# Kernel optimization log

Hardware: AMD Instinct MI355X
Metric: run time of the kernel (lower is better)

Reference implementation:

```python
import jax, jax.numpy as jnp
import numpy as np

B, N, C, CI = 2, 8192, 128, 128
K_SAMP, K_NN = 120, 30  # sampling_ratio, nn_nb
GN_GROUPS, GN_CH = 2, 128
EPS = 1e-5


def setup_inputs() -> dict:
    key = jax.random.key(0)
    ks = jax.random.split(key, 7)
    return {
        "points": jax.random.normal(ks[0], (B, N, 3), jnp.float32),
        "feature": jax.random.normal(ks[1], (B, N, C), jnp.float32),
        "instance_feature": jax.random.normal(ks[2], (B, N, CI), jnp.float32),
        "kpam_w1": jax.random.normal(ks[3], (K_NN, K_NN), jnp.float32) * 0.1,
        "kpam_w2": jax.random.normal(ks[4], (K_NN, K_NN), jnp.float32) * 0.1,
        "conv_w": jax.random.normal(ks[5], (128, 131), jnp.float32) * 0.05,
        "gn_gamma": jnp.ones((GN_CH,), jnp.float32),
        "gn_beta": jnp.zeros((GN_CH,), jnp.float32),
        "mlp_w": jax.random.normal(ks[6], (3, 256), jnp.float32) * 0.05,
        "mlp_b": jnp.zeros((3,), jnp.float32),
    }


def _key_indices(n):
    # replicate torch module: np.random.seed(1234); shuffle(arange(N)); take first 120
    rs = np.random.RandomState(1234)
    l = np.arange(n)
    rs.shuffle(l)
    return jnp.asarray(l[:K_SAMP])


def reference(points, feature, instance_feature, kpam_w1, kpam_w2,
              conv_w, gn_gamma, gn_beta, mlp_w, mlp_b):
    Bv, Nv, _ = points.shape
    idx = _key_indices(Nv)                              # [120] static indices
    key_points = points[:, idx]                         # [B,120,3]
    feat_s = feature[:, idx]                            # [B,120,128]
    inst_s = instance_feature[:, idx]                   # [B,120,CI]

    # cos_dist: -(1 - cos) == cos - 1
    fn = instance_feature / jnp.linalg.norm(instance_feature, axis=-1, keepdims=True)
    gn = inst_s / jnp.linalg.norm(inst_s, axis=-1, keepdims=True)
    dist = jnp.einsum('bnc,bkc->bnk', fn, gn) - 1.0     # [B,N,120]

    topk_dist, topk_idx = jax.lax.top_k(dist, K_NN)     # [B,N,30]

    gather = jax.vmap(lambda tab, ix: tab[ix])          # tab [120,D], ix [N,30]
    topk_kp = gather(key_points, topk_idx)              # [B,N,30,3]
    topk_feat = gather(feat_s, topk_idx)                # [B,N,30,128]

    direction = topk_kp - points[:, :, None, :]         # [B,N,30,3]
    x = jnp.concatenate([topk_feat, direction], axis=3) # [B,N,30,131]

    # KPAM: two 1x1 conv1d over k-channel of topk_dist, softmax over k
    a = jax.nn.relu(jnp.einsum('bnk,ok->bno', topk_dist, kpam_w1))
    a = jnp.einsum('bno,po->bnp', a, kpam_w2)
    attn = jax.nn.softmax(a, axis=2)[..., None]         # [B,N,30,1]
    fa = attn * x                                       # [B,N,30,131]

    # conv1: 1x1 Conv2d 131->128 on layout [B,131,30,N]
    y = jnp.einsum('bnkc,oc->bokn', fa, conv_w)         # [B,128,30,N]

    # GroupNorm(2, 128)
    yg = y.reshape(Bv, GN_GROUPS, GN_CH // GN_GROUPS, K_NN, Nv)
    mu = yg.mean(axis=(2, 3, 4), keepdims=True)
    var = yg.var(axis=(2, 3, 4), keepdims=True)
    yg = (yg - mu) * jax.lax.rsqrt(var + EPS)
    y = yg.reshape(Bv, GN_CH, K_NN, Nv)
    y = y * gn_gamma[None, :, None, None] + gn_beta[None, :, None, None]
    y = jnp.where(y >= 0, y, 0.2 * y)                   # LeakyReLU(0.2)

    y = y.max(axis=2)                                   # max over k -> [B,128,N]
    feat_cat = jnp.concatenate([y, feature.transpose(0, 2, 1)], axis=1)  # [B,256,N]

    offsets = jnp.einsum('bcn,oc->bon', feat_cat, mlp_w) + mlp_b[None, :, None]
    return offsets  # [B,3,N]
```

## Files before the change

### kernel.cpp

```cpp
#include <hip/hip_runtime.h>

#define Bv   2
#define Nv   8192
#define Cv   128
#define KSv  120
#define KNNv 30

namespace mtns {
struct MTState { unsigned mt[624]; int mti; };
constexpr void mt_seed(MTState& s, unsigned seed) {
  for (int pos = 0; pos < 624; ++pos) {
    s.mt[pos] = seed;
    seed = 1812433253u * (seed ^ (seed >> 30)) + (unsigned)pos + 1u;
  }
  s.mti = 624;
}
constexpr unsigned mt_next(MTState& s) {
  if (s.mti >= 624) {
    for (int i = 0; i < 624; ++i) {
      unsigned y = (s.mt[i] & 0x80000000u) | (s.mt[(i + 1) % 624] & 0x7fffffffu);
      unsigned v = s.mt[(i + 397) % 624] ^ (y >> 1);
      s.mt[i] = (y & 1u) ? (v ^ 0x9908b0dfu) : v;
    }
    s.mti = 0;
  }
  unsigned y = s.mt[s.mti++];
  y ^= y >> 11;
  y ^= (y << 7) & 0x9d2c5680u;
  y ^= (y << 15) & 0xefc60000u;
  y ^= y >> 18;
  return y;
}
struct IdxTable { int v[KSv]; };
constexpr IdxTable make_idx() {
  MTState st{};
  mt_seed(st, 1234u);
  int arr[Nv] = {};
  for (int i = 0; i < Nv; ++i) arr[i] = i;
  for (int i = Nv - 1; i > 0; --i) {
    unsigned mask = (unsigned)i;
    mask |= mask >> 1; mask |= mask >> 2; mask |= mask >> 4;
    mask |= mask >> 8; mask |= mask >> 16;
    unsigned j = 0;
    do { j = mt_next(st) & mask; } while (j > (unsigned)i);
    int tmp = arr[i]; arr[i] = arr[(int)j]; arr[(int)j] = tmp;
  }
  IdxTable out{};
  for (int k = 0; k < KSv; ++k) out.v[k] = arr[k];
  return out;
}
}

__constant__ mtns::IdxTable IDX = mtns::make_idx();

__device__ __forceinline__ float wave_sum(float v) {
  #pragma unroll
  for (int m = 32; m; m >>= 1) v += __shfl_xor(v, m);
  return v;
}

__device__ __forceinline__ float opaque(float x) {
  asm volatile("" : "+v"(x));
  return x;
}

__device__ __forceinline__ float rdf(float v, int k) {
  return __int_as_float(__builtin_amdgcn_readlane(__float_as_int(v), k));
}
__device__ __forceinline__ int rdi(int v, int k) {
  return __builtin_amdgcn_readlane(v, k);
}

__device__ __forceinline__ float npyv_reduce(const float4* a) {
  float4 h0, h1, h;
  h0.x = a[0].x + a[2].x; h0.y = a[0].y + a[2].y;
  h0.z = a[0].z + a[2].z; h0.w = a[0].w + a[2].w;
  h1.x = a[1].x + a[3].x; h1.y = a[1].y + a[3].y;
  h1.z = a[1].z + a[3].z; h1.w = a[1].w + a[3].w;
  h.x = h0.x + h1.x; h.y = h0.y + h1.y; h.z = h0.z + h1.z; h.w = h0.w + h1.w;
  float sx = h.x + h.z;
  float sy = h.y + h.w;
  return sx + sy;
}

__global__ void k0_prepare(const float* __restrict__ points,
                           const float* __restrict__ feature,
                           const float* __restrict__ inst,
                           const float* __restrict__ conv_w,
                           float* __restrict__ gn32W,
                           float* __restrict__ GW,
                           int* __restrict__ counter) {
  int bk = blockIdx.x;
  int b = bk / KSv, kp = bk % KSv;
  int jg = IDX.v[kp];
  int t = threadIdx.x;
  if (bk == 0 && t == 0) *counter = 0;
  __shared__ float featS[Cv];
  __shared__ float rowS[Cv];
  __shared__ float ptS[3];
  __shared__ float nAcc[8];
  __shared__ float nrmSh;
  long rowi = (long)b * Nv + jg;
  float iv = inst[rowi * Cv + t];
  rowS[t] = iv;
  featS[t] = feature[rowi * Cv + t];
  if (t < 3) ptS[t] = points[rowi * 3 + t];
  __syncthreads();
  if (t < 8) {
    float x0 = rowS[t];
    float acc = opaque(x0 * x0);
    #pragma unroll
    for (int i = 1; i < 16; ++i) {
      float xv = rowS[8 * i + t];
      acc = acc + opaque(xv * xv);
    }
    nAcc[t] = acc;
  }
  __syncthreads();
  if (t == 0) {
    float res = ((nAcc[0] + nAcc[1]) + (nAcc[2] + nAcc[3])) +
                ((nAcc[4] + nAcc[5]) + (nAcc[6] + nAcc[7]));
    nrmSh = sqrtf(res);
  }
  __syncthreads();
  gn32W[(b * KSv + kp) * Cv + t] = iv / nrmSh;
  const float* cw = conv_w + t * 131;
  float acc = 0.f;
  #pragma unroll 8
  for (int c = 0; c < Cv; ++c) acc = fmaf(featS[c], cw[c], acc);
  acc = fmaf(ptS[0], cw[128], fmaf(ptS[1], cw[129], fmaf(ptS[2], cw[130], acc)));
  GW[(b * KSv + kp) * Cv + t] = acc;
}

__global__ __launch_bounds__(512, 4) void k2_main(
    const float* __restrict__ points,
    const float* __restrict__ inst,
    const float* __restrict__ w1,
    const float* __restrict__ w2,
    const float* __restrict__ conv_w,
    const float* __restrict__ gamma,
    const float* __restrict__ gn32,
    const float* __restrict__ GW,
    float* __restrict__ Msel,
    float2* __restrict__ part,
    int* __restrict__ counter,
    float2* __restrict__ stats) {
  __shared__ float4 gnS[KSv * 32];
  __shared__ float sc[8 * 512];
  __shared__ float2 partS[16];
  __shared__ int lastFlag;

  int bid = blockIdx.x;
  int b = bid >> 9;
  int chunk = bid & 511;
  int tid = threadIdx.x;
  int w = tid >> 6, l = tid & 63;

  const float4* gnG = (const float4*)(gn32 + (long)b * KSv * Cv);
  for (int i = tid; i < KSv * 32; i += 512) {
    int kp = i >> 5, c4 = i & 31;
    gnS[kp * 32 + (c4 ^ (kp & 31))] = gnG[i];
  }
  __syncthreads();

  float* wb = sc + w * 512;
  float* fnA = wb;
  float* fnB = wb + 128;
  float* dsA = wb + 256;
  float* dsB = wb + 384;
  float* tvA = dsA; int* tiA = (int*)(dsA + 32);
  float* tvB = dsB; int* tiB = (int*)(dsB + 32);

  int c0 = 2 * l;
  int nA = chunk * 16 + 2 * w;
  long rowA = (long)b * Nv + nA;
  long rowB = rowA + 1;
  const float* Gb = GW + (long)b * KSv * Cv;
  const float NINF = -__builtin_inff();

  float2 ivA = *(const float2*)(inst + rowA * Cv + c0);
  float2 ivB = *(const float2*)(inst + rowB * Cv + c0);
  ((float2*)fnA)[l] = ivA;
  ((float2*)fnB)[l] = ivB;
  __builtin_amdgcn_wave_barrier();

  float acc = 0.f;
  if (l < 16) {
    const float* xr = (l < 8) ? fnA : fnB;
    int j = l & 7;
    float x0 = xr[j];
    acc = opaque(x0 * x0);
    #pragma unroll
    for (int i = 1; i < 16; ++i) {
      float xv = xr[8 * i + j];
      acc = acc + opaque(xv * xv);
    }
  }
  float nrmA = sqrtf(((rdf(acc, 0) + rdf(acc, 1)) + (rdf(acc, 2) + rdf(acc, 3))) +
                     ((rdf(acc, 4) + rdf(acc, 5)) + (rdf(acc, 6) + rdf(acc, 7))));
  float nrmB = sqrtf(((rdf(acc, 8) + rdf(acc, 9)) + (rdf(acc, 10) + rdf(acc, 11))) +
                     ((rdf(acc, 12) + rdf(acc, 13)) + (rdf(acc, 14) + rdf(acc, 15))));
  __builtin_amdgcn_wave_barrier();
  float2 fA2, fB2;
  fA2.x = ivA.x / nrmA; fA2.y = ivA.y / nrmA;
  fB2.x = ivB.x / nrmB; fB2.y = ivB.y / nrmB;
  ((float2*)fnA)[l] = fA2;
  ((float2*)fnB)[l] = fB2;
  __builtin_amdgcn_wave_barrier();

  const float4* fA4 = (const float4*)fnA;
  const float4* fB4 = (const float4*)fnB;
  int sw = l & 31;
  const float4* g0r = gnS + l * 32;
  int r1 = 64 + l; if (r1 > KSv - 1) r1 = KSv - 1;
  const float4* g1r = gnS + r1 * 32;
  float4 aA0[4], aA1[4], aB0[4], aB1[4];
  #pragma unroll
  for (int i = 0; i < 4; ++i) {
    aA0[i] = float4{0,0,0,0}; aA1[i] = float4{0,0,0,0};
    aB0[i] = float4{0,0,0,0}; aB1[i] = float4{0,0,0,0};
  }
  #pragma unroll 4
  for (int c4 = 0; c4 < 32; ++c4) {
    float4 fa = fA4[c4];
    float4 fb = fB4[c4];
    float4 g0 = g0r[c4 ^ sw];
    float4 g1 = g1r[c4 ^ sw];
    int m = c4 & 3;
    aA0[m].x = fmaf(g0.x, fa.x, aA0[m].x); aA0[m].y = fmaf(g0.y, fa.y, aA0[m].y);
    aA0[m].z = fmaf(g0.z, fa.z, aA0[m].z); aA0[m].w = fmaf(g0.w, fa.w, aA0[m].w);
    aB0[m].x = fmaf(g0.x, fb.x, aB0[m].x); aB0[m].y = fmaf(g0.y, fb.y, aB0[m].y);
    aB0[m].z = fmaf(g0.z, fb.z, aB0[m].z); aB0[m].w = fmaf(g0.w, fb.w, aB0[m].w);
    aA1[m].x = fmaf(g1.x, fa.x, aA1[m].x); aA1[m].y = fmaf(g1.y, fa.y, aA1[m].y);
    aA1[m].z = fmaf(g1.z, fa.z, aA1[m].z); aA1[m].w = fmaf(g1.w, fa.w, aA1[m].w);
    aB1[m].x = fmaf(g1.x, fb.x, aB1[m].x); aB1[m].y = fmaf(g1.y, fb.y, aB1[m].y);
    aB1[m].z = fmaf(g1.z, fb.z, aB1[m].z); aB1[m].w = fmaf(g1.w, fb.w, aB1[m].w);
  }
  float d0A = npyv_reduce(aA0) - 1.0f;
  float d1A = npyv_reduce(aA1) - 1.0f;
  float d0B = npyv_reduce(aB0) - 1.0f;
  float d1B = npyv_reduce(aB1) - 1.0f;

  dsA[l] = d0A;
  dsB[l] = d0B;
  if (l < 56) { dsA[64 + l] = d1A; dsB[64 + l] = d1B; }
  __builtin_amdgcn_wave_barrier();

  float d1Ar = (l < 56) ? d1A : NINF;
  float d1Br = (l < 56) ? d1B : NINF;
  int rk0A = 0, rk1A = 0, rk0B = 0, rk1B = 0;
  const float4* dvA = (const float4*)dsA;
  const float4* dvB = (const float4*)dsB;
  int t1 = 64 + l;
  #pragma unroll 5
  for (int j4 = 0; j4 < KSv / 4; ++j4) {
    float4 wA = dvA[j4];
    float4 wB = dvB[j4];
    int base = j4 * 4;
    rk0A += (wA.x > d0A) || (wA.x == d0A && (base + 0) < l);
    rk0A += (wA.y > d0A) || (wA.y == d0A && (base + 1) < l);
    rk0A += (wA.z > d0A) || (wA.z == d0A && (base + 2) < l);
    rk0A += (wA.w > d0A) || (wA.w == d0A && (base + 3) < l);
    rk1A += (wA.x > d1Ar) || (wA.x == d1Ar && (base + 0) < t1);
    rk1A += (wA.y > d1Ar) || (wA.y == d1Ar && (base + 1) < t1);
    rk1A += (wA.z > d1Ar) || (wA.z == d1Ar && (base + 2) < t1);
    rk1A += (wA.w > d1Ar) || (wA.w == d1Ar && (base + 3) < t1);
    rk0B += (wB.x > d0B) || (wB.x == d0B && (base + 0) < l);
    rk0B += (wB.y > d0B) || (wB.y == d0B && (base + 1) < l);
    rk0B += (wB.z > d0B) || (wB.z == d0B && (base + 2) < l);
    rk0B += (wB.w > d0B) || (wB.w == d0B && (base + 3) < l);
    rk1B += (wB.x > d1Br) || (wB.x == d1Br && (base + 0) < t1);
    rk1B += (wB.y > d1Br) || (wB.y == d1Br && (base + 1) < t1);
    rk1B += (wB.z > d1Br) || (wB.z == d1Br && (base + 2) < t1);
    rk1B += (wB.w > d1Br) || (wB.w == d1Br && (base + 3) < t1);
  }
  __builtin_amdgcn_wave_barrier();
  if (rk0A < KNNv) { tvA[rk0A] = d0A; tiA[rk0A] = l; }
  if (l < 56 && rk1A < KNNv) { tvA[rk1A] = d1A; tiA[rk1A] = t1; }
  if (rk0B < KNNv) { tvB[rk0B] = d0B; tiB[rk0B] = l; }
  if (l < 56 && rk1B < KNNv) { tvB[rk1B] = d1B; tiB[rk1B] = t1; }
  __builtin_amdgcn_wave_barrier();
  float mytvA = 0.f, mytvB = 0.f;
  int mytiA = 0, mytiB = 0;
  if (l < KNNv) {
    mytvA = tvA[l]; mytiA = tiA[l];
    mytvB = tvB[l]; mytiB = tiB[l];
  }

  float aA = 0.f, aB = 0.f;
  if (l < KNNv) {
    const float* w1r = w1 + l * KNNv;
    #pragma unroll 6
    for (int k = 0; k < KNNv; ++k) {
      float w1k = w1r[k];
      aA = fmaf(rdf(mytvA, k), w1k, aA);
      aB = fmaf(rdf(mytvB, k), w1k, aB);
    }
    aA = fmaxf(aA, 0.f);
    aB = fmaxf(aB, 0.f);
  }
  float a2A = NINF, a2B = NINF;
  if (l < KNNv) {
    const float* w2r = w2 + l * KNNv;
    float sA2 = 0.f, sB2 = 0.f;
    #pragma unroll 6
    for (int o = 0; o < KNNv; ++o) {
      float w2o = w2r[o];
      sA2 = fmaf(rdf(aA, o), w2o, sA2);
      sB2 = fmaf(rdf(aB, o), w2o, sB2);
    }
    a2A = sA2; a2B = sB2;
  }

  float mA = a2A, mB = a2B;
  #pragma unroll
  for (int msk = 32; msk; msk >>= 1) {
    mA = fmaxf(mA, __shfl_xor(mA, msk));
    mB = fmaxf(mB, __shfl_xor(mB, msk));
  }
  float evA = (l < KNNv) ? __expf(a2A - mA) : 0.f;
  float evB = (l < KNNv) ? __expf(a2B - mB) : 0.f;
  float invA = 1.0f / wave_sum(evA);
  float invB = 1.0f / wave_sum(evB);
  float atpA = evA * invA;
  float atpB = evB * invB;

  float pA0 = points[rowA * 3 + 0], pA1 = points[rowA * 3 + 1],
        pA2 = points[rowA * 3 + 2];
  float pB0 = points[rowB * 3 + 0], pB1 = points[rowB * 3 + 1],
        pB2 = points[rowB * 3 + 2];
  int c1 = c0 + 1;
  float cwa0 = conv_w[c0 * 131 + 128], cwb0 = conv_w[c0 * 131 + 129],
        cwc0 = conv_w[c0 * 131 + 130];
  float cwa1 = conv_w[c1 * 131 + 128], cwb1 = conv_w[c1 * 131 + 129],
        cwc1 = conv_w[c1 * 131 + 130];
  float pwA0 = fmaf(pA0, cwa0, fmaf(pA1, cwb0, pA2 * cwc0));
  float pwA1 = fmaf(pA0, cwa1, fmaf(pA1, cwb1, pA2 * cwc1));
  float pwB0 = fmaf(pB0, cwa0, fmaf(pB1, cwb0, pB2 * cwc0));
  float pwB1 = fmaf(pB0, cwa1, fmaf(pB1, cwb1, pB2 * cwc1));
  float mxA0 = NINF, mnA0 = -NINF, mxA1 = NINF, mnA1 = -NINF;
  float mxB0 = NINF, mnB0 = -NINF, mxB1 = NINF, mnB1 = -NINF;
  float sA = 0.f, qA = 0.f, sB = 0.f, qB = 0.f;
  #pragma unroll 5
  for (int k = 0; k < KNNv; ++k) {
    float akA = rdf(atpA, k);
    float akB = rdf(atpB, k);
    int jkA = rdi(mytiA, k);
    int jkB = rdi(mytiB, k);
    float2 gA = *(const float2*)(Gb + jkA * Cv + c0);
    float2 gB = *(const float2*)(Gb + jkB * Cv + c0);
    float yA0 = akA * (gA.x - pwA0);
    float yA1 = akA * (gA.y - pwA1);
    float yB0 = akB * (gB.x - pwB0);
    float yB1 = akB * (gB.y - pwB1);
    mxA0 = fmaxf(mxA0, yA0); mnA0 = fminf(mnA0, yA0);
    mxA1 = fmaxf(mxA1, yA1); mnA1 = fminf(mnA1, yA1);
    mxB0 = fmaxf(mxB0, yB0); mnB0 = fminf(mnB0, yB0);
    mxB1 = fmaxf(mxB1, yB1); mnB1 = fminf(mnB1, yB1);
    sA += yA0 + yA1;
    qA = fmaf(yA0, yA0, fmaf(yA1, yA1, qA));
    sB += yB0 + yB1;
    qB = fmaf(yB0, yB0, fmaf(yB1, yB1, qB));
  }
  float ga0 = gamma[c0], ga1 = gamma[c1];
  float2 mselA, mselB;
  mselA.x = (ga0 >= 0.f) ? mxA0 : mnA0;
  mselA.y = (ga1 >= 0.f) ? mxA1 : mnA1;
  mselB.x = (ga0 >= 0.f) ? mxB0 : mnB0;
  mselB.y = (ga1 >= 0.f) ? mxB1 : mnB1;
  *(float2*)(Msel + rowA * Cv + c0) = mselA;
  *(float2*)(Msel + rowB * Cv + c0) = mselB;

  float sg = sA + sB, qg = qA + qB;
  #pragma unroll
  for (int msk = 16; msk; msk >>= 1) {
    sg += __shfl_xor(sg, msk);
    qg += __shfl_xor(qg, msk);
  }
  if ((l & 31) == 0) partS[w * 2 + (l >> 5)] = make_float2(sg, qg);
  __syncthreads();
  if (tid == 0) {
    float s0 = 0.f, q0 = 0.f, s1 = 0.f, q1 = 0.f;
    #pragma unroll
    for (int wv = 0; wv < 8; ++wv) {
      s0 += partS[wv * 2].x;     q0 += partS[wv * 2].y;
      s1 += partS[wv * 2 + 1].x; q1 += partS[wv * 2 + 1].y;
    }
    part[bid * 2 + 0] = make_float2(s0, q0);
    part[bid * 2 + 1] = make_float2(s1, q1);
    __threadfence();
    int old = atomicAdd(counter, 1);
    lastFlag = (old == (int)gridDim.x - 1);
  }
  __syncthreads();
  if (lastFlag && w < 4) {
    int bb = w >> 1, g = w & 1;
    double s = 0.0, q = 0.0;
    #pragma unroll
    for (int i = 0; i < 8; ++i) {
      float2 p = part[(bb * 512 + l + 64 * i) * 2 + g];
      s += (double)p.x;
      q += (double)p.y;
    }
    #pragma unroll
    for (int msk = 32; msk; msk >>= 1) {
      s += __shfl_xor(s, msk);
      q += __shfl_xor(q, msk);
    }
    if (l == 0) {
      const double cnt = 64.0 * 30.0 * 8192.0;
      double mu = s / cnt;
      double var = q / cnt - mu * mu;
      stats[bb * 2 + g] = make_float2((float)mu, (float)(1.0 / sqrt(var + 1e-5)));
    }
  }
}

__global__ __launch_bounds__(256) void k4_out(
    const float* __restrict__ feature,
    const float* __restrict__ gamma,
    const float* __restrict__ beta,
    const float* __restrict__ mlp_w,
    const float* __restrict__ mlp_b,
    const float* __restrict__ Msel,
    const float2* __restrict__ stats,
    float* __restrict__ out) {
  int rr = threadIdx.x >> 7;
  int t = threadIdx.x & 127;
  long row = (long)blockIdx.x * 2 + rr;
  int b = (int)(row >> 13), n = (int)(row & (Nv - 1));
  int g = t >> 6;
  float2 st = stats[b * 2 + g];
  float gam = gamma[t], bet = beta[t];
  float M = Msel[row * Cv + t];
  float yv = fmaf((M - st.x) * st.y, gam, bet);
  yv = (yv >= 0.f) ? yv : 0.2f * yv;
  float fv = feature[row * Cv + t];
  float o0 = yv * mlp_w[0 * 256 + t] + fv * mlp_w[0 * 256 + 128 + t];
  float o1 = yv * mlp_w[1 * 256 + t] + fv * mlp_w[1 * 256 + 128 + t];
  float o2 = yv * mlp_w[2 * 256 + t] + fv * mlp_w[2 * 256 + 128 + t];
  o0 = wave_sum(o0);
  o1 = wave_sum(o1);
  o2 = wave_sum(o2);
  __shared__ float red[2][2][3];
  if ((t & 63) == 0) {
    red[rr][t >> 6][0] = o0; red[rr][t >> 6][1] = o1; red[rr][t >> 6][2] = o2;
  }
  __syncthreads();
  if (t < 3)
    out[(long)b * 3 * Nv + (long)t * Nv + n] =
        red[rr][0][t] + red[rr][1][t] + mlp_b[t];
}

extern "C" void kernel_launch(void* const* d_in, const int* in_sizes, int n_in,
                              void* d_out, int out_size, void* d_ws, size_t ws_size,
                              hipStream_t stream) {
  const float* points  = (const float*)d_in[0];
  const float* feature = (const float*)d_in[1];
  const float* inst    = (const float*)d_in[2];
  const float* w1      = (const float*)d_in[3];
  const float* w2      = (const float*)d_in[4];
  const float* conv_w  = (const float*)d_in[5];
  const float* gamma   = (const float*)d_in[6];
  const float* beta    = (const float*)d_in[7];
  const float* mlp_w   = (const float*)d_in[8];
  const float* mlp_b   = (const float*)d_in[9];
  float* out = (float*)d_out;

  char* ws = (char*)d_ws;
  float* gn32   = (float*)(ws);
  float* GW     = (float*)(ws + 122880);
  float* Msel   = (float*)(ws + 245760);
  float2* part  = (float2*)(ws + 8634368);
  int* counter  = (int*)(ws + 8650752);
  float2* stats = (float2*)(ws + 8650816);

  k0_prepare<<<dim3(Bv * KSv), dim3(128), 0, stream>>>(points, feature, inst,
                                                       conv_w, gn32, GW, counter);
  k2_main<<<dim3(1024), dim3(512), 0, stream>>>(points, inst, w1, w2, conv_w,
                                                gamma, gn32, GW, Msel, part,
                                                counter, stats);
  k4_out<<<dim3(Bv * Nv / 2), dim3(256), 0, stream>>>(feature, gamma, beta,
                                                      mlp_w, mlp_b, Msel,
                                                      stats, out);
}
```

Measured before the change: 172.9 us.

## Fuse prepare, main and output kernels into one cooperative grid-synced kernel

Merges the three launches into a single cooperative kernel of 256 blocks that uses grid.sync between the key-point preparation, the main top-k/attention/conv phase, and the GroupNorm+MLP output phase. Each block now handles 64 points in four passes, keeps the selected max/min values in shared memory instead of writing Msel to global memory, and computes its GroupNorm stats redundantly. Top-k ranking is rewritten to compare packed 64-bit sortable keys via readlane. This removes launch overhead and the Msel round trip, but lowers the grid to 256 blocks at two blocks per CU and adds two grid-wide barriers.

```diff
diff --git a/kernel.cpp b/kernel.cpp
--- a/kernel.cpp
+++ b/kernel.cpp
@@ -1,4 +1,7 @@
 #include <hip/hip_runtime.h>
+#include <hip/hip_cooperative_groups.h>
+
+namespace cg = cooperative_groups;
 
 #define Bv   2
 #define Nv   8192
@@ -70,6 +73,18 @@
 __device__ __forceinline__ int rdi(int v, int k) {
   return __builtin_amdgcn_readlane(v, k);
 }
+__device__ __forceinline__ unsigned long long rdull(unsigned long long v, int k) {
+  unsigned lo = (unsigned)__builtin_amdgcn_readlane((int)(unsigned)(v & 0xFFFFFFFFull), k);
+  unsigned hi = (unsigned)__builtin_amdgcn_readlane((int)(unsigned)(v >> 32), k);
+  return (((unsigned long long)hi) << 32) | lo;
+}
+
+__device__ __forceinline__ unsigned long long mkkey(float d, int t) {
+  unsigned u = __float_as_uint(d);
+  unsigned m = (unsigned)((int)u >> 31);
+  unsigned o = u ^ (m | 0x80000000u);
+  return (((unsigned long long)o) << 7) | (unsigned)(119 - t);
+}
 
 __device__ __forceinline__ float npyv_reduce(const float4* a) {
   float4 h0, h1, h;
@@ -83,79 +98,81 @@
   return sx + sy;
 }
 
-__global__ void k0_prepare(const float* __restrict__ points,
-                           const float* __restrict__ feature,
-                           const float* __restrict__ inst,
-                           const float* __restrict__ conv_w,
-                           float* __restrict__ gn32W,
-                           float* __restrict__ GW,
-                           int* __restrict__ counter) {
-  int bk = blockIdx.x;
-  int b = bk / KSv, kp = bk % KSv;
-  int jg = IDX.v[kp];
-  int t = threadIdx.x;
-  if (bk == 0 && t == 0) *counter = 0;
-  __shared__ float featS[Cv];
-  __shared__ float rowS[Cv];
-  __shared__ float ptS[3];
-  __shared__ float nAcc[8];
-  __shared__ float nrmSh;
-  long rowi = (long)b * Nv + jg;
-  float iv = inst[rowi * Cv + t];
-  rowS[t] = iv;
-  featS[t] = feature[rowi * Cv + t];
-  if (t < 3) ptS[t] = points[rowi * 3 + t];
-  __syncthreads();
-  if (t < 8) {
-    float x0 = rowS[t];
-    float acc = opaque(x0 * x0);
-    #pragma unroll
-    for (int i = 1; i < 16; ++i) {
-      float xv = rowS[8 * i + t];
-      acc = acc + opaque(xv * xv);
-    }
-    nAcc[t] = acc;
-  }
-  __syncthreads();
-  if (t == 0) {
-    float res = ((nAcc[0] + nAcc[1]) + (nAcc[2] + nAcc[3])) +
-                ((nAcc[4] + nAcc[5]) + (nAcc[6] + nAcc[7]));
-    nrmSh = sqrtf(res);
-  }
-  __syncthreads();
-  gn32W[(b * KSv + kp) * Cv + t] = iv / nrmSh;
-  const float* cw = conv_w + t * 131;
-  float acc = 0.f;
-  #pragma unroll 8
-  for (int c = 0; c < Cv; ++c) acc = fmaf(featS[c], cw[c], acc);
-  acc = fmaf(ptS[0], cw[128], fmaf(ptS[1], cw[129], fmaf(ptS[2], cw[130], acc)));
-  GW[(b * KSv + kp) * Cv + t] = acc;
-}
-
-__global__ __launch_bounds__(512, 4) void k2_main(
+__global__ __launch_bounds__(512, 2) void k_all(
     const float* __restrict__ points,
+    const float* __restrict__ feature,
     const float* __restrict__ inst,
     const float* __restrict__ w1,
     const float* __restrict__ w2,
     const float* __restrict__ conv_w,
     const float* __restrict__ gamma,
-    const float* __restrict__ gn32,
-    const float* __restrict__ GW,
-    float* __restrict__ Msel,
+    const float* __restrict__ beta,
+    const float* __restrict__ mlp_w,
+    const float* __restrict__ mlp_b,
+    float* __restrict__ gn32,
+    float* __restrict__ GW,
     float2* __restrict__ part,
-    int* __restrict__ counter,
-    float2* __restrict__ stats) {
+    float* __restrict__ out) {
   __shared__ float4 gnS[KSv * 32];
-  __shared__ float sc[8 * 512];
+  __shared__ float sc[8 * 384];
+  __shared__ float2 mselS[8][8][64];
   __shared__ float2 partS[16];
-  __shared__ int lastFlag;
+  __shared__ float2 statsS[2];
 
   int bid = blockIdx.x;
-  int b = bid >> 9;
-  int chunk = bid & 511;
   int tid = threadIdx.x;
   int w = tid >> 6, l = tid & 63;
-
+  cg::grid_group grid = cg::this_grid();
+
+  if (bid < Bv * KSv) {
+    int b0 = bid / KSv, kp = bid % KSv;
+    int jg = IDX.v[kp];
+    float* rowS = sc;
+    float* featS = sc + 128;
+    float* ptS = sc + 256;
+    float* nAcc = sc + 260;
+    float* nrmP = sc + 268;
+    long rowi = (long)b0 * Nv + jg;
+    if (tid < Cv) {
+      rowS[tid] = inst[rowi * Cv + tid];
+      featS[tid] = feature[rowi * Cv + tid];
+      if (tid < 3) ptS[tid] = points[rowi * 3 + tid];
+    }
+    __syncthreads();
+    if (tid < 8) {
+      float x0 = rowS[tid];
+      float acc = opaque(x0 * x0);
+      #pragma unroll
+      for (int i = 1; i < 16; ++i) {
+        float xv = rowS[8 * i + tid];
+        acc = acc + opaque(xv * xv);
+      }
+      nAcc[tid] = acc;
+    }
+    __syncthreads();
+    if (tid == 0) {
+      float res = ((nAcc[0] + nAcc[1]) + (nAcc[2] + nAcc[3])) +
+                  ((nAcc[4] + nAcc[5]) + (nAcc[6] + nAcc[7]));
+      nrmP[0] = sqrtf(res);
+    }
+    __syncthreads();
+    if (tid < Cv) {
+      float iv = rowS[tid];
+      gn32[(b0 * KSv + kp) * Cv + tid] = iv / nrmP[0];
+      const float* cw = conv_w + tid * 131;
+      float acc = 0.f;
+      #pragma unroll 8
+      for (int c = 0; c < Cv; ++c) acc = fmaf(featS[c], cw[c], acc);
+      acc = fmaf(ptS[0], cw[128],
+                 fmaf(ptS[1], cw[129], fmaf(ptS[2], cw[130], acc)));
+      GW[(b0 * KSv + kp) * Cv + tid] = acc;
+    }
+  }
+  __threadfence();
+  grid.sync();
+
+  int b = bid >> 7;
+  int blocal = bid & 127;
   const float4* gnG = (const float4*)(gn32 + (long)b * KSv * Cv);
   for (int i = tid; i < KSv * 32; i += 512) {
     int kp = i >> 5, c4 = i & 31;
@@ -163,215 +180,200 @@
   }
   __syncthreads();
 
-  float* wb = sc + w * 512;
+  float* wb = sc + w * 384;
   float* fnA = wb;
   float* fnB = wb + 128;
-  float* dsA = wb + 256;
-  float* dsB = wb + 384;
-  float* tvA = dsA; int* tiA = (int*)(dsA + 32);
-  float* tvB = dsB; int* tiB = (int*)(dsB + 32);
-
-  int c0 = 2 * l;
-  int nA = chunk * 16 + 2 * w;
-  long rowA = (long)b * Nv + nA;
-  long rowB = rowA + 1;
-  const float* Gb = GW + (long)b * KSv * Cv;
-  const float NINF = -__builtin_inff();
-
-  float2 ivA = *(const float2*)(inst + rowA * Cv + c0);
-  float2 ivB = *(const float2*)(inst + rowB * Cv + c0);
-  ((float2*)fnA)[l] = ivA;
-  ((float2*)fnB)[l] = ivB;
-  __builtin_amdgcn_wave_barrier();
-
-  float acc = 0.f;
-  if (l < 16) {
-    const float* xr = (l < 8) ? fnA : fnB;
-    int j = l & 7;
-    float x0 = xr[j];
-    acc = opaque(x0 * x0);
-    #pragma unroll
-    for (int i = 1; i < 16; ++i) {
-      float xv = xr[8 * i + j];
-      acc = acc + opaque(xv * xv);
-    }
-  }
-  float nrmA = sqrtf(((rdf(acc, 0) + rdf(acc, 1)) + (rdf(acc, 2) + rdf(acc, 3))) +
-                     ((rdf(acc, 4) + rdf(acc, 5)) + (rdf(acc, 6) + rdf(acc, 7))));
-  float nrmB = sqrtf(((rdf(acc, 8) + rdf(acc, 9)) + (rdf(acc, 10) + rdf(acc, 11))) +
-                     ((rdf(acc, 12) + rdf(acc, 13)) + (rdf(acc, 14) + rdf(acc, 15))));
-  __builtin_amdgcn_wave_barrier();
-  float2 fA2, fB2;
-  fA2.x = ivA.x / nrmA; fA2.y = ivA.y / nrmA;
-  fB2.x = ivB.x / nrmB; fB2.y = ivB.y / nrmB;
-  ((float2*)fnA)[l] = fA2;
-  ((float2*)fnB)[l] = fB2;
-  __builtin_amdgcn_wave_barrier();
-
-  const float4* fA4 = (const float4*)fnA;
-  const float4* fB4 = (const float4*)fnB;
-  int sw = l & 31;
-  const float4* g0r = gnS + l * 32;
-  int r1 = 64 + l; if (r1 > KSv - 1) r1 = KSv - 1;
-  const float4* g1r = gnS + r1 * 32;
-  float4 aA0[4], aA1[4], aB0[4], aB1[4];
-  #pragma unroll
-  for (int i = 0; i < 4; ++i) {
-    aA0[i] = float4{0,0,0,0}; aA1[i] = float4{0,0,0,0};
-    aB0[i] = float4{0,0,0,0}; aB1[i] = float4{0,0,0,0};
-  }
-  #pragma unroll 4
-  for (int c4 = 0; c4 < 32; ++c4) {
-    float4 fa = fA4[c4];
-    float4 fb = fB4[c4];
-    float4 g0 = g0r[c4 ^ sw];
-    float4 g1 = g1r[c4 ^ sw];
-    int m = c4 & 3;
-    aA0[m].x = fmaf(g0.x, fa.x, aA0[m].x); aA0[m].y = fmaf(g0.y, fa.y, aA0[m].y);
-    aA0[m].z = fmaf(g0.z, fa.z, aA0[m].z); aA0[m].w = fmaf(g0.w, fa.w, aA0[m].w);
-    aB0[m].x = fmaf(g0.x, fb.x, aB0[m].x); aB0[m].y = fmaf(g0.y, fb.y, aB0[m].y);
-    aB0[m].z = fmaf(g0.z, fb.z, aB0[m].z); aB0[m].w = fmaf(g0.w, fb.w, aB0[m].w);
-    aA1[m].x = fmaf(g1.x, fa.x, aA1[m].x); aA1[m].y = fmaf(g1.y, fa.y, aA1[m].y);
-    aA1[m].z = fmaf(g1.z, fa.z, aA1[m].z); aA1[m].w = fmaf(g1.w, fa.w, aA1[m].w);
-    aB1[m].x = fmaf(g1.x, fb.x, aB1[m].x); aB1[m].y = fmaf(g1.y, fb.y, aB1[m].y);
-    aB1[m].z = fmaf(g1.z, fb.z, aB1[m].z); aB1[m].w = fmaf(g1.w, fb.w, aB1[m].w);
-  }
-  float d0A = npyv_reduce(aA0) - 1.0f;
-  float d1A = npyv_reduce(aA1) - 1.0f;
-  float d0B = npyv_reduce(aB0) - 1.0f;
-  float d1B = npyv_reduce(aB1) - 1.0f;
-
-  dsA[l] = d0A;
-  dsB[l] = d0B;
-  if (l < 56) { dsA[64 + l] = d1A; dsB[64 + l] = d1B; }
-  __builtin_amdgcn_wave_barrier();
-
-  float d1Ar = (l < 56) ? d1A : NINF;
-  float d1Br = (l < 56) ? d1B : NINF;
-  int rk0A = 0, rk1A = 0, rk0B = 0, rk1B = 0;
-  const float4* dvA = (const float4*)dsA;
-  const float4* dvB = (const float4*)dsB;
-  int t1 = 64 + l;
-  #pragma unroll 5
-  for (int j4 = 0; j4 < KSv / 4; ++j4) {
-    float4 wA = dvA[j4];
-    float4 wB = dvB[j4];
-    int base = j4 * 4;
-    rk0A += (wA.x > d0A) || (wA.x == d0A && (base + 0) < l);
-    rk0A += (wA.y > d0A) || (wA.y == d0A && (base + 1) < l);
-    rk0A += (wA.z > d0A) || (wA.z == d0A && (base + 2) < l);
-    rk0A += (wA.w > d0A) || (wA.w == d0A && (base + 3) < l);
-    rk1A += (wA.x > d1Ar) || (wA.x == d1Ar && (base + 0) < t1);
-    rk1A += (wA.y > d1Ar) || (wA.y == d1Ar && (base + 1) < t1);
-    rk1A += (wA.z > d1Ar) || (wA.z == d1Ar && (base + 2) < t1);
-    rk1A += (wA.w > d1Ar) || (wA.w == d1Ar && (base + 3) < t1);
-    rk0B += (wB.x > d0B) || (wB.x == d0B && (base + 0) < l);
-    rk0B += (wB.y > d0B) || (wB.y == d0B && (base + 1) < l);
-    rk0B += (wB.z > d0B) || (wB.z == d0B && (base + 2) < l);
-    rk0B += (wB.w > d0B) || (wB.w == d0B && (base + 3) < l);
-    rk1B += (wB.x > d1Br) || (wB.x == d1Br && (base + 0) < t1);
-    rk1B += (wB.y > d1Br) || (wB.y == d1Br && (base + 1) < t1);
-    rk1B += (wB.z > d1Br) || (wB.z == d1Br && (base + 2) < t1);
-    rk1B += (wB.w > d1Br) || (wB.w == d1Br && (base + 3) < t1);
-  }
-  __builtin_amdgcn_wave_barrier();
-  if (rk0A < KNNv) { tvA[rk0A] = d0A; tiA[rk0A] = l; }
-  if (l < 56 && rk1A < KNNv) { tvA[rk1A] = d1A; tiA[rk1A] = t1; }
-  if (rk0B < KNNv) { tvB[rk0B] = d0B; tiB[rk0B] = l; }
-  if (l < 56 && rk1B < KNNv) { tvB[rk1B] = d1B; tiB[rk1B] = t1; }
-  __builtin_amdgcn_wave_barrier();
-  float mytvA = 0.f, mytvB = 0.f;
-  int mytiA = 0, mytiB = 0;
-  if (l < KNNv) {
-    mytvA = tvA[l]; mytiA = tiA[l];
-    mytvB = tvB[l]; mytiB = tiB[l];
-  }
-
-  float aA = 0.f, aB = 0.f;
-  if (l < KNNv) {
-    const float* w1r = w1 + l * KNNv;
-    #pragma unroll 6
-    for (int k = 0; k < KNNv; ++k) {
-      float w1k = w1r[k];
-      aA = fmaf(rdf(mytvA, k), w1k, aA);
-      aB = fmaf(rdf(mytvB, k), w1k, aB);
-    }
-    aA = fmaxf(aA, 0.f);
-    aB = fmaxf(aB, 0.f);
-  }
-  float a2A = NINF, a2B = NINF;
-  if (l < KNNv) {
-    const float* w2r = w2 + l * KNNv;
-    float sA2 = 0.f, sB2 = 0.f;
-    #pragma unroll 6
-    for (int o = 0; o < KNNv; ++o) {
-      float w2o = w2r[o];
-      sA2 = fmaf(rdf(aA, o), w2o, sA2);
-      sB2 = fmaf(rdf(aB, o), w2o, sB2);
-    }
-    a2A = sA2; a2B = sB2;
-  }
-
-  float mA = a2A, mB = a2B;
-  #pragma unroll
-  for (int msk = 32; msk; msk >>= 1) {
-    mA = fmaxf(mA, __shfl_xor(mA, msk));
-    mB = fmaxf(mB, __shfl_xor(mB, msk));
-  }
-  float evA = (l < KNNv) ? __expf(a2A - mA) : 0.f;
-  float evB = (l < KNNv) ? __expf(a2B - mB) : 0.f;
-  float invA = 1.0f / wave_sum(evA);
-  float invB = 1.0f / wave_sum(evB);
-  float atpA = evA * invA;
-  float atpB = evB * invB;
-
-  float pA0 = points[rowA * 3 + 0], pA1 = points[rowA * 3 + 1],
-        pA2 = points[rowA * 3 + 2];
-  float pB0 = points[rowB * 3 + 0], pB1 = points[rowB * 3 + 1],
-        pB2 = points[rowB * 3 + 2];
-  int c1 = c0 + 1;
+  float* tvA = wb + 256; int* tiA = (int*)(wb + 288);
+  float* tvB = wb + 320; int* tiB = (int*)(wb + 352);
+
+  int c0 = 2 * l, c1 = 2 * l + 1;
+  float ga0 = gamma[c0], ga1 = gamma[c1];
   float cwa0 = conv_w[c0 * 131 + 128], cwb0 = conv_w[c0 * 131 + 129],
         cwc0 = conv_w[c0 * 131 + 130];
   float cwa1 = conv_w[c1 * 131 + 128], cwb1 = conv_w[c1 * 131 + 129],
         cwc1 = conv_w[c1 * 131 + 130];
-  float pwA0 = fmaf(pA0, cwa0, fmaf(pA1, cwb0, pA2 * cwc0));
-  float pwA1 = fmaf(pA0, cwa1, fmaf(pA1, cwb1, pA2 * cwc1));
-  float pwB0 = fmaf(pB0, cwa0, fmaf(pB1, cwb0, pB2 * cwc0));
-  float pwB1 = fmaf(pB0, cwa1, fmaf(pB1, cwb1, pB2 * cwc1));
-  float mxA0 = NINF, mnA0 = -NINF, mxA1 = NINF, mnA1 = -NINF;
-  float mxB0 = NINF, mnB0 = -NINF, mxB1 = NINF, mnB1 = -NINF;
-  float sA = 0.f, qA = 0.f, sB = 0.f, qB = 0.f;
-  #pragma unroll 5
-  for (int k = 0; k < KNNv; ++k) {
-    float akA = rdf(atpA, k);
-    float akB = rdf(atpB, k);
-    int jkA = rdi(mytiA, k);
-    int jkB = rdi(mytiB, k);
-    float2 gA = *(const float2*)(Gb + jkA * Cv + c0);
-    float2 gB = *(const float2*)(Gb + jkB * Cv + c0);
-    float yA0 = akA * (gA.x - pwA0);
-    float yA1 = akA * (gA.y - pwA1);
-    float yB0 = akB * (gB.x - pwB0);
-    float yB1 = akB * (gB.y - pwB1);
-    mxA0 = fmaxf(mxA0, yA0); mnA0 = fminf(mnA0, yA0);
-    mxA1 = fmaxf(mxA1, yA1); mnA1 = fminf(mnA1, yA1);
-    mxB0 = fmaxf(mxB0, yB0); mnB0 = fminf(mnB0, yB0);
-    mxB1 = fmaxf(mxB1, yB1); mnB1 = fminf(mnB1, yB1);
-    sA += yA0 + yA1;
-    qA = fmaf(yA0, yA0, fmaf(yA1, yA1, qA));
-    sB += yB0 + yB1;
-    qB = fmaf(yB0, yB0, fmaf(yB1, yB1, qB));
-  }
-  float ga0 = gamma[c0], ga1 = gamma[c1];
-  float2 mselA, mselB;
-  mselA.x = (ga0 >= 0.f) ? mxA0 : mnA0;
-  mselA.y = (ga1 >= 0.f) ? mxA1 : mnA1;
-  mselB.x = (ga0 >= 0.f) ? mxB0 : mnB0;
-  mselB.y = (ga1 >= 0.f) ? mxB1 : mnB1;
-  *(float2*)(Msel + rowA * Cv + c0) = mselA;
-  *(float2*)(Msel + rowB * Cv + c0) = mselB;
-
-  float sg = sA + sB, qg = qA + qB;
+  const float* Gb = GW + (long)b * KSv * Cv;
+  const float NINF = -__builtin_inff();
+  float sAcc = 0.f, qAcc = 0.f;
+
+  #pragma clang loop unroll(disable)
+  for (int pe = 0; pe < 4; ++pe) {
+    int nA = blocal * 64 + w * 8 + pe * 2;
+    long rowA = (long)b * Nv + nA;
+    long rowB = rowA + 1;
+    __builtin_amdgcn_wave_barrier();
+    float2 ivA = *(const float2*)(inst + rowA * Cv + c0);
+    float2 ivB = *(const float2*)(inst + rowB * Cv + c0);
+    ((float2*)fnA)[l] = ivA;
+    ((float2*)fnB)[l] = ivB;
+    __builtin_amdgcn_wave_barrier();
+    float acc = 0.f;
+    if (l < 16) {
+      const float* xr = (l < 8) ? fnA : fnB;
+      int j = l & 7;
+      float x0 = xr[j];
+      acc = opaque(x0 * x0);
+      #pragma unroll
+      for (int i = 1; i < 16; ++i) {
+        float xv = xr[8 * i + j];
+        acc = acc + opaque(xv * xv);
+      }
+    }
+    float nrmA = sqrtf(((rdf(acc, 0) + rdf(acc, 1)) + (rdf(acc, 2) + rdf(acc, 3))) +
+                       ((rdf(acc, 4) + rdf(acc, 5)) + (rdf(acc, 6) + rdf(acc, 7))));
+    float nrmB = sqrtf(((rdf(acc, 8) + rdf(acc, 9)) + (rdf(acc, 10) + rdf(acc, 11))) +
+                       ((rdf(acc, 12) + rdf(acc, 13)) + (rdf(acc, 14) + rdf(acc, 15))));
+    __builtin_amdgcn_wave_barrier();
+    float2 fA2, fB2;
+    fA2.x = ivA.x / nrmA; fA2.y = ivA.y / nrmA;
+    fB2.x = ivB.x / nrmB; fB2.y = ivB.y / nrmB;
+    ((float2*)fnA)[l] = fA2;
+    ((float2*)fnB)[l] = fB2;
+    __builtin_amdgcn_wave_barrier();
+
+    const float4* fA4 = (const float4*)fnA;
+    const float4* fB4 = (const float4*)fnB;
+    int sw = l & 31;
+    const float4* g0r = gnS + l * 32;
+    int r1 = 64 + l; if (r1 > KSv - 1) r1 = KSv - 1;
+    const float4* g1r = gnS + r1 * 32;
+    float4 aA0[4], aA1[4], aB0[4], aB1[4];
+    #pragma unroll
+    for (int i = 0; i < 4; ++i) {
+      aA0[i] = float4{0,0,0,0}; aA1[i] = float4{0,0,0,0};
+      aB0[i] = float4{0,0,0,0}; aB1[i] = float4{0,0,0,0};
+    }
+    #pragma unroll 4
+    for (int c4 = 0; c4 < 32; ++c4) {
+      float4 fa = fA4[c4];
+      float4 fb = fB4[c4];
+      float4 g0 = g0r[c4 ^ sw];
+      float4 g1 = g1r[c4 ^ sw];
+      int m = c4 & 3;
+      aA0[m].x = fmaf(g0.x, fa.x, aA0[m].x); aA0[m].y = fmaf(g0.y, fa.y, aA0[m].y);
+      aA0[m].z = fmaf(g0.z, fa.z, aA0[m].z); aA0[m].w = fmaf(g0.w, fa.w, aA0[m].w);
+      aB0[m].x = fmaf(g0.x, fb.x, aB0[m].x); aB0[m].y = fmaf(g0.y, fb.y, aB0[m].y);
+      aB0[m].z = fmaf(g0.z, fb.z, aB0[m].z); aB0[m].w = fmaf(g0.w, fb.w, aB0[m].w);
+      aA1[m].x = fmaf(g1.x, fa.x, aA1[m].x); aA1[m].y = fmaf(g1.y, fa.y, aA1[m].y);
+      aA1[m].z = fmaf(g1.z, fa.z, aA1[m].z); aA1[m].w = fmaf(g1.w, fa.w, aA1[m].w);
+      aB1[m].x = fmaf(g1.x, fb.x, aB1[m].x); aB1[m].y = fmaf(g1.y, fb.y, aB1[m].y);
+      aB1[m].z = fmaf(g1.z, fb.z, aB1[m].z); aB1[m].w = fmaf(g1.w, fb.w, aB1[m].w);
+    }
+    float d0A = npyv_reduce(aA0) - 1.0f;
+    float d1A = npyv_reduce(aA1) - 1.0f;
+    float d0B = npyv_reduce(aB0) - 1.0f;
+    float d1B = npyv_reduce(aB1) - 1.0f;
+
+    unsigned long long kA0 = mkkey(d0A, l);
+    unsigned long long kB0 = mkkey(d0B, l);
+    unsigned long long kA1 = (l < 56) ? mkkey(d1A, 64 + l) : 0ull;
+    unsigned long long kB1 = (l < 56) ? mkkey(d1B, 64 + l) : 0ull;
+
+    int rkA0 = 0, rkA1 = 0, rkB0 = 0, rkB1 = 0;
+    for (int j = 0; j < 64; ++j) {
+      unsigned long long a0 = rdull(kA0, j);
+      unsigned long long a1 = rdull(kA1, j);
+      unsigned long long b0 = rdull(kB0, j);
+      unsigned long long b1 = rdull(kB1, j);
+      rkA0 += (a0 > kA0); rkA0 += (a1 > kA0);
+      rkA1 += (a0 > kA1); rkA1 += (a1 > kA1);
+      rkB0 += (b0 > kB0); rkB0 += (b1 > kB0);
+      rkB1 += (b0 > kB1); rkB1 += (b1 > kB1);
+    }
+    if (rkA0 < KNNv) { tvA[rkA0] = d0A; tiA[rkA0] = l; }
+    if (l < 56 && rkA1 < KNNv) { tvA[rkA1] = d1A; tiA[rkA1] = 64 + l; }
+    if (rkB0 < KNNv) { tvB[rkB0] = d0B; tiB[rkB0] = l; }
+    if (l < 56 && rkB1 < KNNv) { tvB[rkB1] = d1B; tiB[rkB1] = 64 + l; }
+    __builtin_amdgcn_wave_barrier();
+    float mytvA = 0.f, mytvB = 0.f;
+    int mytiA = 0, mytiB = 0;
+    if (l < KNNv) {
+      mytvA = tvA[l]; mytiA = tiA[l];
+      mytvB = tvB[l]; mytiB = tiB[l];
+    }
+
+    float aA = 0.f, aB = 0.f;
+    if (l < KNNv) {
+      const float* w1r = w1 + l * KNNv;
+      #pragma unroll 6
+      for (int k = 0; k < KNNv; ++k) {
+        float w1k = w1r[k];
+        aA = fmaf(rdf(mytvA, k), w1k, aA);
+        aB = fmaf(rdf(mytvB, k), w1k, aB);
+      }
+      aA = fmaxf(aA, 0.f);
+      aB = fmaxf(aB, 0.f);
+    }
+    float a2A = NINF, a2B = NINF;
+    if (l < KNNv) {
+      const float* w2r = w2 + l * KNNv;
+      float sA2 = 0.f, sB2 = 0.f;
+      #pragma unroll 6
+      for (int o = 0; o < KNNv; ++o) {
+        float w2o = w2r[o];
+        sA2 = fmaf(rdf(aA, o), w2o, sA2);
+        sB2 = fmaf(rdf(aB, o), w2o, sB2);
+      }
+      a2A = sA2; a2B = sB2;
+    }
+
+    float mA = a2A, mB = a2B;
+    #pragma unroll
+    for (int msk = 32; msk; msk >>= 1) {
+      mA = fmaxf(mA, __shfl_xor(mA, msk));
+      mB = fmaxf(mB, __shfl_xor(mB, msk));
+    }
+    float evA = (l < KNNv) ? __expf(a2A - mA) : 0.f;
+    float evB = (l < KNNv) ? __expf(a2B - mB) : 0.f;
+    float invA = 1.0f / wave_sum(evA);
+    float invB = 1.0f / wave_sum(evB);
+    float atpA = evA * invA;
+    float atpB = evB * invB;
+
+    float pA0 = points[rowA * 3 + 0], pA1 = points[rowA * 3 + 1],
+          pA2 = points[rowA * 3 + 2];
+    float pB0 = points[rowB * 3 + 0], pB1 = points[rowB * 3 + 1],
+          pB2 = points[rowB * 3 + 2];
+    float pwA0 = fmaf(pA0, cwa0, fmaf(pA1, cwb0, pA2 * cwc0));
+    float pwA1 = fmaf(pA0, cwa1, fmaf(pA1, cwb1, pA2 * cwc1));
+    float pwB0 = fmaf(pB0, cwa0, fmaf(pB1, cwb0, pB2 * cwc0));
+    float pwB1 = fmaf(pB0, cwa1, fmaf(pB1, cwb1, pB2 * cwc1));
+    float mxA0 = NINF, mnA0 = -NINF, mxA1 = NINF, mnA1 = -NINF;
+    float mxB0 = NINF, mnB0 = -NINF, mxB1 = NINF, mnB1 = -NINF;
+    float sA = 0.f, qA = 0.f, sB = 0.f, qB = 0.f;
+    #pragma unroll 5
+    for (int k = 0; k < KNNv; ++k) {
+      float akA = rdf(atpA, k);
+      float akB = rdf(atpB, k);
+      int jkA = rdi(mytiA, k);
+      int jkB = rdi(mytiB, k);
+      float2 gA = *(const float2*)(Gb + jkA * Cv + c0);
+      float2 gB = *(const float2*)(Gb + jkB * Cv + c0);
+      float yA0 = akA * (gA.x - pwA0);
+      float yA1 = akA * (gA.y - pwA1);
+      float yB0 = akB * (gB.x - pwB0);
+      float yB1 = akB * (gB.y - pwB1);
+      mxA0 = fmaxf(mxA0, yA0); mnA0 = fminf(mnA0, yA0);
+      mxA1 = fmaxf(mxA1, yA1); mnA1 = fminf(mnA1, yA1);
+      mxB0 = fmaxf(mxB0, yB0); mnB0 = fminf(mnB0, yB0);
+      mxB1 = fmaxf(mxB1, yB1); mnB1 = fminf(mnB1, yB1);
+      sA += yA0 + yA1;
+      qA = fmaf(yA0, yA0, fmaf(yA1, yA1, qA));
+      sB += yB0 + yB1;
+      qB = fmaf(yB0, yB0, fmaf(yB1, yB1, qB));
+    }
+    float2 mselA, mselB;
+    mselA.x = (ga0 >= 0.f) ? mxA0 : mnA0;
+    mselA.y = (ga1 >= 0.f) ? mxA1 : mnA1;
+    mselB.x = (ga0 >= 0.f) ? mxB0 : mnB0;
+    mselB.y = (ga1 >= 0.f) ? mxB1 : mnB1;
+    mselS[w][pe * 2 + 0][l] = mselA;
+    mselS[w][pe * 2 + 1][l] = mselB;
+    sAcc += sA + sB;
+    qAcc += qA + qB;
+  }
+
+  float sg = sAcc, qg = qAcc;
   #pragma unroll
   for (int msk = 16; msk; msk >>= 1) {
     sg += __shfl_xor(sg, msk);
@@ -388,68 +390,62 @@
     }
     part[bid * 2 + 0] = make_float2(s0, q0);
     part[bid * 2 + 1] = make_float2(s1, q1);
-    __threadfence();
-    int old = atomicAdd(counter, 1);
-    lastFlag = (old == (int)gridDim.x - 1);
+  }
+  __threadfence();
+  grid.sync();
+
+  if (w == 0) {
+    #pragma unroll
+    for (int g = 0; g < 2; ++g) {
+      float2 pa0 = part[((b * 128) + l) * 2 + g];
+      float2 pa1 = part[((b * 128) + 64 + l) * 2 + g];
+      double s = (double)pa0.x + (double)pa1.x;
+      double q = (double)pa0.y + (double)pa1.y;
+      #pragma unroll
+      for (int msk = 32; msk; msk >>= 1) {
+        s += __shfl_xor(s, msk);
+        q += __shfl_xor(q, msk);
+      }
+      if (l == 0) {
+        const double cnt = 64.0 * 30.0 * 8192.0;
+        double mu = s / cnt;
+        double var = q / cnt - mu * mu;
+        statsS[g] = make_float2((float)mu, (float)(1.0 / sqrt(var + 1e-5)));
+      }
+    }
   }
   __syncthreads();
-  if (lastFlag && w < 4) {
-    int bb = w >> 1, g = w & 1;
-    double s = 0.0, q = 0.0;
-    #pragma unroll
-    for (int i = 0; i < 8; ++i) {
-      float2 p = part[(bb * 512 + l + 64 * i) * 2 + g];
-      s += (double)p.x;
-      q += (double)p.y;
-    }
-    #pragma unroll
-    for (int msk = 32; msk; msk >>= 1) {
-      s += __shfl_xor(s, msk);
-      q += __shfl_xor(q, msk);
-    }
-    if (l == 0) {
-      const double cnt = 64.0 * 30.0 * 8192.0;
-      double mu = s / cnt;
-      double var = q / cnt - mu * mu;
-      stats[bb * 2 + g] = make_float2((float)mu, (float)(1.0 / sqrt(var + 1e-5)));
-    }
-  }
-}
-
-__global__ __launch_bounds__(256) void k4_out(
-    const float* __restrict__ feature,
-    const float* __restrict__ gamma,
-    const float* __restrict__ beta,
-    const float* __restrict__ mlp_w,
-    const float* __restrict__ mlp_b,
-    const float* __restrict__ Msel,
-    const float2* __restrict__ stats,
-    float* __restrict__ out) {
-  int rr = threadIdx.x >> 7;
-  int t = threadIdx.x & 127;
-  long row = (long)blockIdx.x * 2 + rr;
-  int b = (int)(row >> 13), n = (int)(row & (Nv - 1));
-  int g = t >> 6;
-  float2 st = stats[b * 2 + g];
-  float gam = gamma[t], bet = beta[t];
-  float M = Msel[row * Cv + t];
-  float yv = fmaf((M - st.x) * st.y, gam, bet);
-  yv = (yv >= 0.f) ? yv : 0.2f * yv;
-  float fv = feature[row * Cv + t];
-  float o0 = yv * mlp_w[0 * 256 + t] + fv * mlp_w[0 * 256 + 128 + t];
-  float o1 = yv * mlp_w[1 * 256 + t] + fv * mlp_w[1 * 256 + 128 + t];
-  float o2 = yv * mlp_w[2 * 256 + t] + fv * mlp_w[2 * 256 + 128 + t];
-  o0 = wave_sum(o0);
-  o1 = wave_sum(o1);
-  o2 = wave_sum(o2);
-  __shared__ float red[2][2][3];
-  if ((t & 63) == 0) {
-    red[rr][t >> 6][0] = o0; red[rr][t >> 6][1] = o1; red[rr][t >> 6][2] = o2;
-  }
-  __syncthreads();
-  if (t < 3)
-    out[(long)b * 3 * Nv + (long)t * Nv + n] =
-        red[rr][0][t] + red[rr][1][t] + mlp_b[t];
+
+  float2 stg = statsS[l >> 5];
+  float bet0 = beta[c0], bet1 = beta[c1];
+  float2 mw0a = *(const float2*)(mlp_w + 0 * 256 + c0);
+  float2 mw1a = *(const float2*)(mlp_w + 1 * 256 + c0);
+  float2 mw2a = *(const float2*)(mlp_w + 2 * 256 + c0);
+  float2 mw0b = *(const float2*)(mlp_w + 0 * 256 + 128 + c0);
+  float2 mw1b = *(const float2*)(mlp_w + 1 * 256 + 128 + c0);
+  float2 mw2b = *(const float2*)(mlp_w + 2 * 256 + 128 + c0);
+  float mb = (l < 3) ? mlp_b[l] : 0.f;
+  #pragma clang loop unroll(disable)
+  for (int r = 0; r < 8; ++r) {
+    int n = blocal * 64 + w * 8 + r;
+    long row = (long)b * Nv + n;
+    float2 ms = mselS[w][r][l];
+    float2 fv = *(const float2*)(feature + row * Cv + c0);
+    float yv0 = fmaf((ms.x - stg.x) * stg.y, ga0, bet0);
+    float yv1 = fmaf((ms.y - stg.x) * stg.y, ga1, bet1);
+    yv0 = (yv0 >= 0.f) ? yv0 : 0.2f * yv0;
+    yv1 = (yv1 >= 0.f) ? yv1 : 0.2f * yv1;
+    float p0 = yv0 * mw0a.x + yv1 * mw0a.y + fv.x * mw0b.x + fv.y * mw0b.y;
+    float p1 = yv0 * mw1a.x + yv1 * mw1a.y + fv.x * mw1b.x + fv.y * mw1b.y;
+    float p2 = yv0 * mw2a.x + yv1 * mw2a.y + fv.x * mw2b.x + fv.y * mw2b.y;
+    float s0 = wave_sum(p0);
+    float s1 = wave_sum(p1);
+    float s2 = wave_sum(p2);
+    if (l < 3) {
+      float sv = (l == 0) ? s0 : ((l == 1) ? s1 : s2);
+      out[(long)b * 3 * Nv + (long)l * Nv + n] = sv + mb;
+    }
+  }
 }
 
 extern "C" void kernel_launch(void* const* d_in, const int* in_sizes, int n_in,
@@ -468,19 +464,15 @@
   float* out = (float*)d_out;
 
   char* ws = (char*)d_ws;
-  float* gn32   = (float*)(ws);
-  float* GW     = (float*)(ws + 122880);
-  float* Msel   = (float*)(ws + 245760);
-  float2* part  = (float2*)(ws + 8634368);
-  int* counter  = (int*)(ws + 8650752);
-  float2* stats = (float2*)(ws + 8650816);
-
-  k0_prepare<<<dim3(Bv * KSv), dim3(128), 0, stream>>>(points, feature, inst,
-                                                       conv_w, gn32, GW, counter);
-  k2_main<<<dim3(1024), dim3(512), 0, stream>>>(points, inst, w1, w2, conv_w,
-                                                gamma, gn32, GW, Msel, part,
-                                                counter, stats);
-  k4_out<<<dim3(Bv * Nv / 2), dim3(256), 0, stream>>>(feature, gamma, beta,
-                                                      mlp_w, mlp_b, Msel,
-                                                      stats, out);
-}
+  float* gn32  = (float*)(ws);
+  float* GW    = (float*)(ws + 122880);
+  float2* part = (float2*)(ws + 245760);
+
+  void* args[] = {
+    (void*)&points, (void*)&feature, (void*)&inst, (void*)&w1, (void*)&w2,
+    (void*)&conv_w, (void*)&gamma, (void*)&beta, (void*)&mlp_w, (void*)&mlp_b,
+    (void*)&gn32, (void*)&GW, (void*)&part, (void*)&out
+  };
+  hipLaunchCooperativeKernel((void*)k_all, dim3(256), dim3(512), args, 0,
+                             stream);
+}
```

Measured after the change: 315.8 us. 1.83x slower.
